# Kernel tuning notes

Measured on AMD Instinct MI355X. Metric: run time of the kernel, lower is better.

The kernel has to match this reference:

```python
import jax, jax.numpy as jnp
import numpy as np

L = 3      # lstm layers
K = 8      # beam size
NEG = -1e30


def _lstm_layers(x, h, c, W_ih, W_hh, b_ih, b_hh):
    # x: [N, H]; h, c: [L, N, H]; W_*: [L, 4H, H]; b_*: [L, 4H]
    hs, cs = [], []
    inp = x
    for l in range(L):
        g = inp @ W_ih[l].T + b_ih[l] + h[l] @ W_hh[l].T + b_hh[l]  # [N, 4H]
        i, f, gg, o = jnp.split(g, 4, axis=-1)  # pytorch gate order i,f,g,o
        c_new = jax.nn.sigmoid(f) * c[l] + jax.nn.sigmoid(i) * jnp.tanh(gg)
        h_new = jax.nn.sigmoid(o) * jnp.tanh(c_new)
        hs.append(h_new); cs.append(c_new)
        inp = h_new
    return inp, jnp.stack(hs), jnp.stack(cs)


def setup_inputs() -> dict:
    key = jax.random.key(0)
    ks = jax.random.split(key, 8)
    T, B, H, C = 64, 128, 256, 256
    s = 0.05  # keep logits/gates in a sane range
    return {
        "x":    jax.random.normal(ks[0], (T, B, H), jnp.float32),
        "emb":  jax.random.normal(ks[1], (C, H), jnp.float32) * s,
        "W_ih": jax.random.normal(ks[2], (L, 4 * H, H), jnp.float32) * s,
        "W_hh": jax.random.normal(ks[3], (L, 4 * H, H), jnp.float32) * s,
        "b_ih": jax.random.normal(ks[4], (L, 4 * H), jnp.float32) * s,
        "b_hh": jax.random.normal(ks[5], (L, 4 * H), jnp.float32) * s,
        "Wp":   jax.random.normal(ks[6], (C, H), jnp.float32) * s,
        "bp":   jax.random.normal(ks[7], (C,), jnp.float32) * s,
    }


def reference(x, emb, W_ih, W_hh, b_ih, b_hh, Wp, bp):
    # Inference (beam-search) branch of AutoregTypeDecoder.forward, with the
    # per-sample Python loop vectorized over the batch (all num_vars == T).
    T, B, H = x.shape
    C = Wp.shape[0]

    # get_rnn_init: one LSTM step on padded_x[0:1] from zero state
    z = jnp.zeros((L, B, H), x.dtype)
    _, h0, c0 = _lstm_layers(x[0], z, z, W_ih, W_hh, b_ih, b_hh)

    # replicate beam dim; only beam 0 is live initially (prefix score 0)
    h = jnp.broadcast_to(h0[:, :, None, :], (L, B, K, H))
    c = jnp.broadcast_to(c0[:, :, None, :], (L, B, K, H))
    state = jnp.broadcast_to(x[0][:, None, :], (B, K, H))
    prefix = jnp.full((B, K), NEG, x.dtype).at[:, 0].set(0.0)
    choices = jnp.zeros((B, K, T), jnp.int32)

    def step(carry, t):
        state, h, c, prefix, choices = carry
        logp = jax.nn.log_softmax(state @ Wp.T + bp, axis=-1)        # [B,K,C]
        joint = (prefix[:, :, None] + logp).reshape(B, K * C)
        prefix_new, idx = jax.lax.top_k(joint, K)                    # [B,K]
        prev = idx // C
        cls = idx % C
        # beam bookkeeping: gather surviving hypotheses
        h2 = jnp.take_along_axis(h, prev[None, :, :, None], axis=2)
        c2 = jnp.take_along_axis(c, prev[None, :, :, None], axis=2)
        choices = jnp.take_along_axis(choices, prev[:, :, None], axis=1)
        choices = choices.at[:, :, t].set(cls.astype(jnp.int32))
        # one LSTM step on the chosen class embeddings (beams folded into batch)
        e = emb[cls].reshape(B * K, H)
        out, h3, c3 = _lstm_layers(e, h2.reshape(L, B * K, H), c2.reshape(L, B * K, H),
                                   W_ih, W_hh, b_ih, b_hh)
        t_next = jnp.minimum(t + 1, T - 1)  # last step's state is never read
        state_new = out.reshape(B, K, H) + x[t_next][:, None, :]
        return (state_new, h3.reshape(L, B, K, H), c3.reshape(L, B, K, H),
                prefix_new, choices), None

    (state, h, c, prefix, choices), _ = jax.lax.scan(
        step, (state, h, c, prefix, choices), jnp.arange(T))
    return choices, prefix  # per-sample beam choices [B,K,T], beam scores [B,K]
```

## Files before the change

### kernel.cpp

```cpp
#include <hip/hip_runtime.h>
#include <math.h>

static constexpr size_t O_EMBW  = 0;
static constexpr size_t O_WPT   = 262144;
static constexpr size_t O_WIHT  = 327680;
static constexpr size_t O_WHHT  = 1114112;
static constexpr size_t O_BIASC = 1900544;
static constexpr size_t O_XCHG  = 1903616;
static constexpr size_t O_FLAGS = 2952192;

typedef float f2 __attribute__((ext_vector_type(2)));
__device__ __forceinline__ f2 fma2(f2 a, f2 b, f2 c){ return __builtin_elementwise_fma(a,b,c); }
__device__ __forceinline__ float sigf(float x){ return 1.0f/(1.0f + expf(-x)); }

__device__ __forceinline__ void astoref(float* p, float v){
  __hip_atomic_store(p, v, __ATOMIC_RELAXED, __HIP_MEMORY_SCOPE_AGENT);
}
__device__ __forceinline__ float aloadf(const float* p){
  return __hip_atomic_load((float*)p, __ATOMIC_RELAXED, __HIP_MEMORY_SCOPE_AGENT);
}

__global__ __launch_bounds__(256) void k_prep(
    const float* __restrict__ Wih, const float* __restrict__ Whh,
    const float* __restrict__ Wp,  const float* __restrict__ bih,
    const float* __restrict__ bhh,
    float* __restrict__ wihT, float* __restrict__ whhT,
    float* __restrict__ WpT, float* __restrict__ biasC,
    float* __restrict__ flagsF)
{
  const int NT = 786432;
  const int TOTAL = 2*NT + 65536 + 3072 + 1024;
  int stride = gridDim.x * blockDim.x;
  for (int i = blockIdx.x*blockDim.x + threadIdx.x; i < TOTAL; i += stride){
    if (i < NT){
      int l = i / 262144, r = i % 262144;
      int row = r >> 8, k = r & 255;
      int g = row >> 8, uu = row & 255;
      wihT[(size_t)l*262144 + (k<<10) + (uu<<2) + g] = Wih[i];
    } else if (i < 2*NT){
      int j = i - NT;
      int l = j / 262144, r = j % 262144;
      int row = r >> 8, k = r & 255;
      int g = row >> 8, uu = row & 255;
      whhT[(size_t)l*262144 + (k<<10) + (uu<<2) + g] = Whh[j];
    } else if (i < 2*NT + 65536){
      int j = i - 2*NT; int c = j >> 8, k = j & 255;
      WpT[(k<<8) + c] = Wp[j];
    } else if (i < 2*NT + 65536 + 3072){
      int j = i - 2*NT - 65536;
      int l = j >> 10; int cg = j & 1023, uu = cg >> 2, g = cg & 3;
      biasC[j] = bih[l*1024 + g*256 + uu] + bhh[l*1024 + g*256 + uu];
    } else {
      flagsF[i - (2*NT + 65536 + 3072)] = 0.0f;
    }
  }
}

__global__ __launch_bounds__(256) void k_embW(
    const float* __restrict__ emb, const float* __restrict__ wih0T,
    const float* __restrict__ bih, const float* __restrict__ bhh,
    float* __restrict__ embW)
{
  const int cls = blockIdx.x, uu = threadIdx.x;
  const float* er = emb + cls*256;
  float a0=0.f,a1=0.f,a2=0.f,a3=0.f;
  for (int k=0;k<256;k++){
    float ev = er[k];
    float4 w = *(const float4*)&wih0T[k*1024 + uu*4];
    a0 = fmaf(ev, w.x, a0); a1 = fmaf(ev, w.y, a1);
    a2 = fmaf(ev, w.z, a2); a3 = fmaf(ev, w.w, a3);
  }
  a0 += bih[uu]       + bhh[uu];
  a1 += bih[256+uu]   + bhh[256+uu];
  a2 += bih[512+uu]   + bhh[512+uu];
  a3 += bih[768+uu]   + bhh[768+uu];
  *(float4*)&embW[cls*1024 + uu*4] = make_float4(a0,a1,a2,a3);
}

__global__
__attribute__((amdgpu_flat_work_group_size(512,512)))
void k_decode(
    const float* __restrict__ x,
    const float* __restrict__ WpT,
    const float* __restrict__ wihT,
    const float* __restrict__ whhT,
    const float* __restrict__ biasC,
    const float* __restrict__ embW,
    const float* __restrict__ bp,
    float* __restrict__ xchg,
    unsigned* __restrict__ flags,
    float* __restrict__ out)
{
  __shared__ float hS[3*2048];
  __shared__ float cS[1024];
  __shared__ float st[2048];
  __shared__ float jnt[6144];
  __shared__ float pfx[8];
  __shared__ float red[8];  __shared__ int redi[8];
  __shared__ float sVal[8]; __shared__ int sPrev[8], sCls[8];
  __shared__ short prevH[512], clsH[512];

  const int tid  = threadIdx.x;
  const int bid  = blockIdx.x;
  const int half = (bid & 7) >> 2;
  const int oh   = half ^ 1;
  const int smp  = ((bid >> 3) << 2) | (bid & 3);
  const int u    = tid & 127;
  const int kq   = tid >> 7;
  const int U    = (half << 7) | u;
  const int or0  = kq*2;
  const int or1  = or0 + 1;
  const int wv   = tid >> 6, lane = tid & 63;

  float* xbase = xchg + (size_t)smp*8192;
  unsigned* fme = flags + smp*8 + half;
  unsigned* fpr = flags + smp*8 + oh;

  float creg[3][2];
  const float bpc = bp[U];

  if (tid < 64) *(float4*)&jnt[2048 + tid*4] = *(const float4*)&x[(size_t)smp*256 + tid*4];
  if (tid < 8)  pfx[tid] = (tid==0) ? 0.0f : -1e30f;
  __syncthreads();
  *(float4*)&st[tid*4] = *(const float4*)&jnt[2048 + (tid&63)*4];

  for (int l=0; l<3; l++){
    if (tid < 128){
      const float* Wg = wihT + (size_t)l*262144;
      float a0=0.f,a1=0.f,a2=0.f,a3=0.f;
      for (int kc=0; kc<256; kc+=4){
        float4 a4 = *(const float4*)&jnt[2048+kc];
        float4 w0 = *(const float4*)&Wg[(size_t)(kc+0)*1024 + U*4];
        float4 w1 = *(const float4*)&Wg[(size_t)(kc+1)*1024 + U*4];
        float4 w2 = *(const float4*)&Wg[(size_t)(kc+2)*1024 + U*4];
        float4 w3 = *(const float4*)&Wg[(size_t)(kc+3)*1024 + U*4];
        a0=fmaf(a4.x,w0.x,a0); a0=fmaf(a4.y,w1.x,a0); a0=fmaf(a4.z,w2.x,a0); a0=fmaf(a4.w,w3.x,a0);
        a1=fmaf(a4.x,w0.y,a1); a1=fmaf(a4.y,w1.y,a1); a1=fmaf(a4.z,w2.y,a1); a1=fmaf(a4.w,w3.y,a1);
        a2=fmaf(a4.x,w0.z,a2); a2=fmaf(a4.y,w1.z,a2); a2=fmaf(a4.z,w2.z,a2); a2=fmaf(a4.w,w3.z,a2);
        a3=fmaf(a4.x,w0.w,a3); a3=fmaf(a4.y,w1.w,a3); a3=fmaf(a4.z,w2.w,a3); a3=fmaf(a4.w,w3.w,a3);
      }
      float4 bs = *(const float4*)&biasC[(l*256+U)*4];
      float gi=a0+bs.x, gg=a2+bs.z, go=a3+bs.w;
      float cn = sigf(gi)*tanhf(gg);
      float hn = sigf(go)*tanhf(cn);
      jnt[tid] = hn; jnt[128+tid] = cn;
    }
    __syncthreads();
    {
      float* xm = xbase + (half*4 + (l+1))*1024;
      float hv = jnt[u], cv = jnt[128+u];
      creg[l][0] = cv; creg[l][1] = cv;
      hS[l*2048 + or0*256 + U] = hv;
      hS[l*2048 + or1*256 + U] = hv;
      astoref(&xm[or0*128 + u], hv);
      astoref(&xm[or1*128 + u], hv);
    }
    __syncthreads();
    if (tid==0){
      __hip_atomic_store(&fme[(l+1)*2], 1u, __ATOMIC_RELAXED, __HIP_MEMORY_SCOPE_AGENT);
      while (__hip_atomic_load(&fpr[(l+1)*2], __ATOMIC_RELAXED, __HIP_MEMORY_SCOPE_AGENT) < 1u)
        __builtin_amdgcn_s_sleep(2);
    }
    __syncthreads();
    {
      const float* xr = xbase + (oh*4 + (l+1))*1024;
      int r = tid>>6, u2 = (tid&63)*2;
      float v0 = aloadf(&xr[r*128+u2]);
      float v1 = aloadf(&xr[r*128+u2+1]);
      hS[l*2048 + r*256 + (oh<<7)+u2]   = v0;
      hS[l*2048 + r*256 + (oh<<7)+u2+1] = v1;
      if (l<2 && r==0){ jnt[2048+(oh<<7)+u2] = v0; jnt[2048+(oh<<7)+u2+1] = v1; }
    }
    if (l<2 && tid<128) jnt[2048 + U] = jnt[tid];
    __syncthreads();
  }

  auto gemm8 = [&](const float* hbaseK, const int* ro, const float* WgK, f2* acc2){
    const float* Wr = WgK + (U<<2);
    float4 wst[2][4];
    #pragma unroll
    for (int s=0; s<2; s++){
      const float* Wn = Wr + (size_t)(s*4)*1024;
      wst[s][0]=*(const float4*)&Wn[0];    wst[s][1]=*(const float4*)&Wn[1024];
      wst[s][2]=*(const float4*)&Wn[2048]; wst[s][3]=*(const float4*)&Wn[3072];
    }
    auto macblk = [&](const float4 wk[4], const float4 a[8]){
      #pragma unroll
      for (int kk=0;kk<4;kk++){
        f2 wlo = {wk[kk].x, wk[kk].y};
        f2 whi = {wk[kk].z, wk[kk].w};
        const float av4[8] = {
          kk==0?a[0].x:(kk==1?a[0].y:(kk==2?a[0].z:a[0].w)),
          kk==0?a[1].x:(kk==1?a[1].y:(kk==2?a[1].z:a[1].w)),
          kk==0?a[2].x:(kk==1?a[2].y:(kk==2?a[2].z:a[2].w)),
          kk==0?a[3].x:(kk==1?a[3].y:(kk==2?a[3].z:a[3].w)),
          kk==0?a[4].x:(kk==1?a[4].y:(kk==2?a[4].z:a[4].w)),
          kk==0?a[5].x:(kk==1?a[5].y:(kk==2?a[5].z:a[5].w)),
          kk==0?a[6].x:(kk==1?a[6].y:(kk==2?a[6].z:a[6].w)),
          kk==0?a[7].x:(kk==1?a[7].y:(kk==2?a[7].z:a[7].w))};
        #pragma unroll
        for (int i=0;i<8;i++){
          f2 av = {av4[i], av4[i]};
          acc2[i*2+0] = fma2(av, wlo, acc2[i*2+0]);
          acc2[i*2+1] = fma2(av, whi, acc2[i*2+1]);
        }
      }
    };
    #pragma unroll 1
    for (int kc=0; kc<56; kc+=8){
      #pragma unroll
      for (int s=0; s<2; s++){
        const int kcur = kc + s*4;
        const float4 wk[4] = {wst[s][0], wst[s][1], wst[s][2], wst[s][3]};
        const float* Wn = Wr + (size_t)(kcur+8)*1024;
        wst[s][0]=*(const float4*)&Wn[0];    wst[s][1]=*(const float4*)&Wn[1024];
        wst[s][2]=*(const float4*)&Wn[2048]; wst[s][3]=*(const float4*)&Wn[3072];
        float4 a[8];
        #pragma unroll
        for (int i=0;i<8;i++) a[i] = *(const float4*)&hbaseK[ro[i] + kcur];
        macblk(wk, a);
      }
    }
    #pragma unroll
    for (int s=0; s<2; s++){
      const int kcur = 56 + s*4;
      const float4 wk[4] = {wst[s][0], wst[s][1], wst[s][2], wst[s][3]};
      float4 a[8];
      #pragma unroll
      for (int i=0;i<8;i++) a[i] = *(const float4*)&hbaseK[ro[i] + kcur];
      macblk(wk, a);
    }
  };

  const int kqb = kq << 6;

  for (int t=0; t<64; t++){
    if (tid==0){
      unsigned want = (unsigned)(t+1);
      while (__hip_atomic_load(&fpr[3*2], __ATOMIC_RELAXED, __HIP_MEMORY_SCOPE_AGENT) < want)
        __builtin_amdgcn_s_sleep(2);
    }
    __syncthreads();
    {
      const float* xr = xbase + (oh*4 + 3)*1024;
      int r = tid>>6, u2 = (tid&63)*2;
      float v0 = aloadf(&xr[r*128+u2]);
      float v1 = aloadf(&xr[r*128+u2+1]);
      hS[2*2048 + r*256 + (oh<<7)+u2]   = v0;
      hS[2*2048 + r*256 + (oh<<7)+u2+1] = v1;
      if (t > 0){
        f2 xv = *(const f2*)&x[(size_t)t*32768 + smp*256 + (oh<<7)+u2];
        st[r*256 + (oh<<7)+u2]   = v0 + xv.x;
        st[r*256 + (oh<<7)+u2+1] = v1 + xv.y;
      }
    }
    __syncthreads();

    {
      const int rq = tid >> 7;
      const float* A0 = st + (rq*2)*256;
      const float* A1 = st + (rq*2+1)*256;
      const float* Wc = WpT + U;
      f2 q01 = {0.f,0.f};
      float wstp[4][4];
      #pragma unroll
      for (int s=0;s<4;s++){
        #pragma unroll
        for (int q=0;q<4;q++) wstp[s][q] = Wc[(s*4+q)*256];
      }
      #pragma unroll 1
      for (int kc=0; kc<240; kc+=16){
        #pragma unroll
        for (int s=0;s<4;s++){
          const int kcur = kc + s*4;
          float w0=wstp[s][0], w1=wstp[s][1], w2=wstp[s][2], w3=wstp[s][3];
          #pragma unroll
          for (int q=0;q<4;q++) wstp[s][q] = Wc[(kcur+16+q)*256];
          float4 a0 = *(const float4*)&A0[kcur];
          float4 a1 = *(const float4*)&A1[kcur];
          q01 = fma2((f2){a0.x,a1.x}, (f2){w0,w0}, q01);
          q01 = fma2((f2){a0.y,a1.y}, (f2){w1,w1}, q01);
          q01 = fma2((f2){a0.z,a1.z}, (f2){w2,w2}, q01);
          q01 = fma2((f2){a0.w,a1.w}, (f2){w3,w3}, q01);
        }
      }
      #pragma unroll
      for (int s=0;s<4;s++){
        const int kcur = 240 + s*4;
        float w0=wstp[s][0], w1=wstp[s][1], w2=wstp[s][2], w3=wstp[s][3];
        float4 a0 = *(const float4*)&A0[kcur];
        float4 a1 = *(const float4*)&A1[kcur];
        q01 = fma2((f2){a0.x,a1.x}, (f2){w0,w0}, q01);
        q01 = fma2((f2){a0.y,a1.y}, (f2){w1,w1}, q01);
        q01 = fma2((f2){a0.z,a1.z}, (f2){w2,w2}, q01);
        q01 = fma2((f2){a0.w,a1.w}, (f2){w3,w3}, q01);
      }
      float v0 = q01.x + bpc, v1 = q01.y + bpc;
      float* xm = xbase + (half*4 + 0)*1024;
      jnt[(rq*2)*256 + U]   = v0;
      jnt[(rq*2+1)*256 + U] = v1;
      astoref(&xm[(rq*2)*128 + u],   v0);
      astoref(&xm[(rq*2+1)*128 + u], v1);
    }
    __syncthreads();
    if (tid==0){
      __hip_atomic_store(&fme[0], (unsigned)(t+1), __ATOMIC_RELAXED, __HIP_MEMORY_SCOPE_AGENT);
      while (__hip_atomic_load(&fpr[0], __ATOMIC_RELAXED, __HIP_MEMORY_SCOPE_AGENT) < (unsigned)(t+1))
        __builtin_amdgcn_s_sleep(2);
    }
    __syncthreads();
    {
      const float* xr = xbase + (oh*4 + 0)*1024;
      int r = tid>>6, c2 = (tid&63)*2;
      jnt[r*256 + (oh<<7) + c2]   = aloadf(&xr[r*128+c2]);
      jnt[r*256 + (oh<<7) + c2+1] = aloadf(&xr[r*128+c2+1]);
    }
    __syncthreads();

    {
      const int kb = wv;
      float4 v = *(const float4*)&jnt[kb*256 + lane*4];
      float m = fmaxf(fmaxf(v.x,v.y),fmaxf(v.z,v.w));
      for (int off=32;off;off>>=1) m = fmaxf(m, __shfl_down(m,off));
      m = __shfl(m, 0);
      double s = exp((double)v.x-(double)m)+exp((double)v.y-(double)m)
               + exp((double)v.z-(double)m)+exp((double)v.w-(double)m);
      for (int off=32;off;off>>=1) s += __shfl_down(s,off);
      s = __shfl(s, 0);
      double lse = log(s);
      float pf = pfx[kb];
      float4 o;
      o.x = (float)((double)v.x - (double)m - lse) + pf;
      o.y = (float)((double)v.y - (double)m - lse) + pf;
      o.z = (float)((double)v.z - (double)m - lse) + pf;
      o.w = (float)((double)v.w - (double)m - lse) + pf;
      *(float4*)&jnt[kb*256+lane*4] = o;
    }
    __syncthreads();

    for (int r=0;r<8;r++){
      float bv = -INFINITY; int bi = 0;
      #pragma unroll
      for (int i=0;i<4;i++){
        int idx = tid + 512*i; float vv = jnt[idx];
        if (vv > bv){ bv=vv; bi=idx; }
      }
      for (int off=32;off;off>>=1){
        float ov = __shfl_down(bv,off); int oi = __shfl_down(bi,off);
        if (ov>bv || (ov==bv && oi<bi)){ bv=ov; bi=oi; }
      }
      if (lane==0){ red[wv]=bv; redi[wv]=bi; }
      __syncthreads();
      if (tid==0){
        float BV=red[0]; int BI=redi[0];
        for (int j=1;j<8;j++) if (red[j]>BV || (red[j]==BV && redi[j]<BI)){BV=red[j];BI=redi[j];}
        sVal[r]=BV; sPrev[r]=BI>>8; sCls[r]=BI&255;
        jnt[BI] = -INFINITY;
      }
      __syncthreads();
    }
    if (tid<8){
      pfx[tid] = sVal[tid];
      prevH[t*8+tid] = (short)sPrev[tid];
      clsH[t*8+tid]  = (short)sCls[tid];
    }
    __syncthreads();

    int rog8[8], rod8[8];
    #pragma unroll
    for (int r=0;r<8;r++){ rog8[r] = sPrev[r]*256; rod8[r] = r*256; }
    const int clr0 = sCls[or0], clr1 = sCls[or1];
    const int pv0  = sPrev[or0], pv1 = sPrev[or1];

    #pragma unroll 1
    for (int l=0; l<3; l++){
      cS[or0*128 + u] = creg[l][0];
      cS[or1*128 + u] = creg[l][1];
      __syncthreads();

      f2 acc2[16];
      #pragma unroll
      for (int i=0;i<16;i++) acc2[i] = (f2){0.f,0.f};
      gemm8(hS + l*2048 + kqb, rog8,
            whhT + (size_t)l*262144 + (size_t)kqb*1024, acc2);
      if (l > 0){
        if (tid==0){
          unsigned want = (unsigned)(t+2);
          while (__hip_atomic_load(&fpr[l*2], __ATOMIC_RELAXED, __HIP_MEMORY_SCOPE_AGENT) < want)
            __builtin_amdgcn_s_sleep(2);
        }
        __syncthreads();
        {
          const float* xr = xbase + (oh*4 + l)*1024;
          int r = tid>>6, u2 = (tid&63)*2;
          hS[(l-1)*2048 + r*256 + (oh<<7)+u2]   = aloadf(&xr[r*128+u2]);
          hS[(l-1)*2048 + r*256 + (oh<<7)+u2+1] = aloadf(&xr[r*128+u2+1]);
        }
        __syncthreads();
        gemm8(hS + (l-1)*2048 + kqb, rod8,
              wihT + (size_t)l*262144 + (size_t)kqb*1024, acc2);
      }

      f2 G0, G1, G2, G3;
      {
        const int dA = (tid ^ 256) * 12;
        const int dB = (tid ^ 128) * 12;
        float4 p0, p1, r0, r1;
        if (kq < 2){
          p0 = make_float4(acc2[8].x, acc2[8].y, acc2[9].x, acc2[9].y);
          p1 = make_float4(acc2[10].x,acc2[10].y,acc2[11].x,acc2[11].y);
        } else {
          p0 = make_float4(acc2[0].x, acc2[0].y, acc2[1].x, acc2[1].y);
          p1 = make_float4(acc2[2].x, acc2[2].y, acc2[3].x, acc2[3].y);
        }
        *(float4*)&jnt[dA] = p0; *(float4*)&jnt[dA+4] = p1;
        __syncthreads();
        r0 = *(const float4*)&jnt[tid*12];
        r1 = *(const float4*)&jnt[tid*12+4];
        if (kq < 2){
          acc2[0] += (f2){r0.x,r0.y}; acc2[1] += (f2){r0.z,r0.w};
          acc2[2] += (f2){r1.x,r1.y}; acc2[3] += (f2){r1.z,r1.w};
        } else {
          acc2[0] = acc2[8]  + (f2){r0.x,r0.y}; acc2[1] = acc2[9]  + (f2){r0.z,r0.w};
          acc2[2] = acc2[10] + (f2){r1.x,r1.y}; acc2[3] = acc2[11] + (f2){r1.z,r1.w};
        }
        __syncthreads();
        if (kq < 2){
          p0 = make_float4(acc2[12].x,acc2[12].y,acc2[13].x,acc2[13].y);
          p1 = make_float4(acc2[14].x,acc2[14].y,acc2[15].x,acc2[15].y);
        } else {
          p0 = make_float4(acc2[4].x, acc2[4].y, acc2[5].x, acc2[5].y);
          p1 = make_float4(acc2[6].x, acc2[6].y, acc2[7].x, acc2[7].y);
        }
        *(float4*)&jnt[dA] = p0; *(float4*)&jnt[dA+4] = p1;
        __syncthreads();
        r0 = *(const float4*)&jnt[tid*12];
        r1 = *(const float4*)&jnt[tid*12+4];
        if (kq < 2){
          acc2[4] += (f2){r0.x,r0.y}; acc2[5] += (f2){r0.z,r0.w};
          acc2[6] += (f2){r1.x,r1.y}; acc2[7] += (f2){r1.z,r1.w};
        } else {
          acc2[4] = acc2[12] + (f2){r0.x,r0.y}; acc2[5] = acc2[13] + (f2){r0.z,r0.w};
          acc2[6] = acc2[14] + (f2){r1.x,r1.y}; acc2[7] = acc2[15] + (f2){r1.z,r1.w};
        }
        __syncthreads();
        if (kq & 1){
          p0 = make_float4(acc2[0].x, acc2[0].y, acc2[1].x, acc2[1].y);
          p1 = make_float4(acc2[2].x, acc2[2].y, acc2[3].x, acc2[3].y);
        } else {
          p0 = make_float4(acc2[4].x, acc2[4].y, acc2[5].x, acc2[5].y);
          p1 = make_float4(acc2[6].x, acc2[6].y, acc2[7].x, acc2[7].y);
        }
        *(float4*)&jnt[dB] = p0; *(float4*)&jnt[dB+4] = p1;
        __syncthreads();
        r0 = *(const float4*)&jnt[tid*12];
        r1 = *(const float4*)&jnt[tid*12+4];
        f2 k0, k1, k2, k3;
        if (kq & 1){ k0=acc2[4]; k1=acc2[5]; k2=acc2[6]; k3=acc2[7]; }
        else       { k0=acc2[0]; k1=acc2[1]; k2=acc2[2]; k3=acc2[3]; }
        G0 = k0 + (f2){r0.x,r0.y};
        G1 = k1 + (f2){r0.z,r0.w};
        G2 = k2 + (f2){r1.x,r1.y};
        G3 = k3 + (f2){r1.z,r1.w};
      }

      {
        const int tn = (t < 63) ? (t+1) : 63;
        float4 b0, b1;
        if (l==0){
          b0 = *(const float4*)&embW[(size_t)clr0*1024 + U*4];
          b1 = *(const float4*)&embW[(size_t)clr1*1024 + U*4];
        } else {
          b0 = *(const float4*)&biasC[(l*256+U)*4];
          b1 = b0;
        }
        float co0 = cS[pv0*128 + u], co1 = cS[pv1*128 + u];
        float gi0 = G0.x + b0.x, gf0 = G0.y + b0.y;
        float gg0 = G1.x + b0.z, go0 = G1.y + b0.w;
        float cn0 = sigf(gf0)*co0 + sigf(gi0)*tanhf(gg0);
        float hn0 = sigf(go0)*tanhf(cn0);
        float gi1 = G2.x + b1.x, gf1 = G2.y + b1.y;
        float gg1 = G3.x + b1.z, go1 = G3.y + b1.w;
        float cn1 = sigf(gf1)*co1 + sigf(gi1)*tanhf(gg1);
        float hn1 = sigf(go1)*tanhf(cn1);
        creg[l][0] = cn0; creg[l][1] = cn1;
        hS[l*2048 + or0*256 + U] = hn0;
        hS[l*2048 + or1*256 + U] = hn1;
        if (l == 2){
          float xv = x[(size_t)tn*32768 + smp*256 + U];
          st[or0*256 + U] = hn0 + xv;
          st[or1*256 + U] = hn1 + xv;
        }
        float* xm = xbase + (half*4 + (l+1))*1024;
        astoref(&xm[or0*128 + u], hn0);
        astoref(&xm[or1*128 + u], hn1);
      }
      __syncthreads();
      if (tid==0)
        __hip_atomic_store(&fme[(l+1)*2], (unsigned)(t+2), __ATOMIC_RELAXED, __HIP_MEMORY_SCOPE_AGENT);
    }
  }

  if (half==0 && tid < 8){
    int e = tid;
    for (int tt=63; tt>=0; --tt){
      out[(size_t)(smp*8+tid)*64 + tt] = (float)clsH[tt*8+e];
      e = (int)prevH[tt*8+e];
    }
    out[65536 + smp*8 + tid] = pfx[tid];
  }
}

extern "C" void kernel_launch(void* const* d_in, const int* in_sizes, int n_in,
                              void* d_out, int out_size, void* d_ws, size_t ws_size,
                              hipStream_t stream)
{
  const float* x   = (const float*)d_in[0];
  const float* emb = (const float*)d_in[1];
  const float* Wih = (const float*)d_in[2];
  const float* Whh = (const float*)d_in[3];
  const float* bih = (const float*)d_in[4];
  const float* bhh = (const float*)d_in[5];
  const float* Wp  = (const float*)d_in[6];
  const float* bp  = (const float*)d_in[7];
  float* ws = (float*)d_ws;

  float* embW  = ws + O_EMBW;
  float* WpT   = ws + O_WPT;
  float* wihT  = ws + O_WIHT;
  float* whhT  = ws + O_WHHT;
  float* biasC = ws + O_BIASC;
  float* xchg  = ws + O_XCHG;
  unsigned* flags = (unsigned*)(ws + O_FLAGS);

  k_prep<<<256,256,0,stream>>>(Wih,Whh,Wp,bih,bhh,wihT,whhT,WpT,biasC, ws + O_FLAGS);
  k_embW<<<256,256,0,stream>>>(emb, wihT, bih, bhh, embW);
  k_decode<<<256,512,0,stream>>>(x, WpT, wihT, whhT, biasC, embW, bp, xchg, flags, (float*)d_out);
}
```

Measured before the change: 4.278 ms.

## Use two-level per-wave top-k and prefetch weights into cache during waits

Replaces the eight block-wide serial argmax passes, each needing two block barriers, with a two-stage scheme. Each wave first picks its own top 8 with shuffles, then one wave merges the 64 candidates. It also adds dummy loads of WpT and of the LSTM weight slices during the spin-wait windows so they are warm in L2/L1 before use, and publishes the progress flag earlier. The prefetch adds memory traffic and register use in exchange for hiding load latency behind the cross-block handshake.

```diff
diff --git a/kernel.cpp b/kernel.cpp
--- a/kernel.cpp
+++ b/kernel.cpp
@@ -96,7 +96,7 @@
   __shared__ float st[2048];
   __shared__ float jnt[6144];
   __shared__ float pfx[8];
-  __shared__ float red[8];  __shared__ int redi[8];
+  __shared__ float cvS[64]; __shared__ int ciS[64];
   __shared__ float sVal[8]; __shared__ int sPrev[8], sCls[8];
   __shared__ short prevH[512], clsH[512];
 
@@ -235,6 +235,16 @@
   const int kqb = kq << 6;
 
   for (int t=0; t<64; t++){
+    if (wv){
+      float sum = 0.f;
+      const float* pp = WpT + (half<<7);
+      #pragma unroll
+      for (int j=0;j<4;j++){
+        int n = tid + (j<<9);
+        sum += pp[((size_t)(n>>3)<<8) + ((n&7)<<4)];
+      }
+      asm volatile("" :: "v"(sum));
+    }
     if (tid==0){
       unsigned want = (unsigned)(t+1);
       while (__hip_atomic_load(&fpr[3*2], __ATOMIC_RELAXED, __HIP_MEMORY_SCOPE_AGENT) < want)
@@ -303,8 +313,22 @@
       astoref(&xm[(rq*2+1)*128 + u], v1);
     }
     __syncthreads();
+    if (tid==0)
+      __hip_atomic_store(&fme[0], (unsigned)(t+1), __ATOMIC_RELAXED, __HIP_MEMORY_SCOPE_AGENT);
+    if (wv){
+      float sum = 0.f;
+      const float* pw = whhT + ((size_t)half<<9);
+      const float* pi = wihT + ((size_t)half<<9);
+      #pragma unroll 4
+      for (int j=0;j<16;j++){
+        int n = tid + (j<<9);
+        size_t off = ((size_t)(n>>5)<<10) + ((n&31)<<4);
+        sum += pw[off] + pw[262144+off] + pw[524288+off]
+             + pi[262144+off] + pi[524288+off];
+      }
+      asm volatile("" :: "v"(sum));
+    }
     if (tid==0){
-      __hip_atomic_store(&fme[0], (unsigned)(t+1), __ATOMIC_RELAXED, __HIP_MEMORY_SCOPE_AGENT);
       while (__hip_atomic_load(&fpr[0], __ATOMIC_RELAXED, __HIP_MEMORY_SCOPE_AGENT) < (unsigned)(t+1))
         __builtin_amdgcn_s_sleep(2);
     }
@@ -338,27 +362,46 @@
     }
     __syncthreads();
 
-    for (int r=0;r<8;r++){
-      float bv = -INFINITY; int bi = 0;
-      #pragma unroll
-      for (int i=0;i<4;i++){
-        int idx = tid + 512*i; float vv = jnt[idx];
-        if (vv > bv){ bv=vv; bi=idx; }
-      }
-      for (int off=32;off;off>>=1){
-        float ov = __shfl_down(bv,off); int oi = __shfl_down(bi,off);
-        if (ov>bv || (ov==bv && oi<bi)){ bv=ov; bi=oi; }
-      }
-      if (lane==0){ red[wv]=bv; redi[wv]=bi; }
-      __syncthreads();
-      if (tid==0){
-        float BV=red[0]; int BI=redi[0];
-        for (int j=1;j<8;j++) if (red[j]>BV || (red[j]==BV && redi[j]<BI)){BV=red[j];BI=redi[j];}
-        sVal[r]=BV; sPrev[r]=BI>>8; sCls[r]=BI&255;
-        jnt[BI] = -INFINITY;
-      }
-      __syncthreads();
-    }
+    {
+      float4 v4 = *(const float4*)&jnt[wv*256 + lane*4];
+      float e0=v4.x, e1=v4.y, e2=v4.z, e3=v4.w;
+      const int ib = wv*256 + lane*4;
+      #pragma unroll 1
+      for (int r=0;r<8;r++){
+        float bv = e0; int bi = ib;
+        if (e1>bv){bv=e1;bi=ib+1;}
+        if (e2>bv){bv=e2;bi=ib+2;}
+        if (e3>bv){bv=e3;bi=ib+3;}
+        #pragma unroll
+        for (int off=32;off;off>>=1){
+          float ov=__shfl_down(bv,off); int oi=__shfl_down(bi,off);
+          if (ov>bv||(ov==bv&&oi<bi)){bv=ov;bi=oi;}
+        }
+        bi=__shfl(bi,0);
+        if (lane==0){ cvS[wv*8+r]=bv; ciS[wv*8+r]=bi; }
+        if (bi==ib)        e0=-INFINITY;
+        else if (bi==ib+1) e1=-INFINITY;
+        else if (bi==ib+2) e2=-INFINITY;
+        else if (bi==ib+3) e3=-INFINITY;
+      }
+    }
+    __syncthreads();
+    if (wv==0){
+      float mv = cvS[lane]; int mi = ciS[lane];
+      #pragma unroll 1
+      for (int r=0;r<8;r++){
+        float bv=mv; int bi=mi;
+        #pragma unroll
+        for (int off=32;off;off>>=1){
+          float ov=__shfl_down(bv,off); int oi=__shfl_down(bi,off);
+          if (ov>bv||(ov==bv&&oi<bi)){bv=ov;bi=oi;}
+        }
+        bv=__shfl(bv,0); bi=__shfl(bi,0);
+        if (lane==0){ sVal[r]=bv; sPrev[r]=bi>>8; sCls[r]=bi&255; }
+        if (mi==bi) mv=-INFINITY;
+      }
+    }
+    __syncthreads();
     if (tid<8){
       pfx[tid] = sVal[tid];
       prevH[t*8+tid] = (short)sPrev[tid];
```

Result: slower. 6.282 ms (+46.9%).
